# Kernel tuning notes

Measured on AMD Instinct MI355X. Metric: run time of the kernel, lower is better.

The kernel has to match this reference:

```python
import jax, jax.numpy as jnp
import numpy as np

EPS = 1e-6
ROPE_BASE = 10000.0


def layer_norm(x, scale, bias):
    mu = jnp.mean(x, axis=-1, keepdims=True)
    var = jnp.mean(jnp.square(x - mu), axis=-1, keepdims=True)
    return (x - mu) * jax.lax.rsqrt(var + EPS) * scale + bias


def make_rope(head_dim, seq_len):
    half = head_dim // 2
    inv_freq = 1.0 / (ROPE_BASE ** (jnp.arange(half, dtype=jnp.float32) / half))
    freqs = jnp.outer(jnp.arange(seq_len, dtype=jnp.float32), inv_freq)  # (T, half)
    cos = jnp.concatenate([jnp.cos(freqs), jnp.cos(freqs)], axis=-1)[:, None, :]  # (T,1,Dh)
    sin = jnp.concatenate([jnp.sin(freqs), jnp.sin(freqs)], axis=-1)[:, None, :]

    def rotate_half(x):
        x1, x2 = x[..., :half], x[..., half:]
        return jnp.concatenate([-x2, x1], axis=-1)

    def apply(q, k):
        return q * cos + rotate_half(q) * sin, k * cos + rotate_half(k) * sin
    return apply


def mha(x, Wq, bq, Wk, bk, Wv, bv, Wo, bo, causal, rope):
    # x: (..., S, D) -> (..., S, D)
    q = jnp.einsum('...sd,dhk->...shk', x, Wq) + bq
    k = jnp.einsum('...sd,dhk->...shk', x, Wk) + bk
    v = jnp.einsum('...sd,dhk->...shk', x, Wv) + bv
    if rope is not None:
        q, k = rope(q, k)
    scale = 1.0 / np.sqrt(q.shape[-1]).astype(np.float32)
    logits = jnp.einsum('...thk,...shk->...hts', q, k) * scale
    if causal:
        S = q.shape[-3]
        mask = jnp.tril(jnp.ones((S, S), dtype=jnp.bool_))
        logits = jnp.where(mask, logits, jnp.finfo(logits.dtype).min)
    probs = jax.nn.softmax(logits, axis=-1)
    o = jnp.einsum('...hts,...shk->...thk', probs, v)
    return jnp.einsum('...thk,hkd->...td', o, Wo) + bo


def setup_inputs() -> dict:
    key = jax.random.key(0)
    B, T, M, D, H, Dh, F = 8, 128, 16, 1024, 16, 64, 4096
    ks = jax.random.split(key, 12)
    s = 0.02
    return {
        'x': jax.random.normal(ks[0], (B, T, M, D), jnp.float32),
        'ln1_scale': jnp.ones((D,), jnp.float32), 'ln1_bias': jnp.zeros((D,), jnp.float32),
        't_Wq': jax.random.normal(ks[1], (D, H, Dh), jnp.float32) * s,
        't_bq': jnp.zeros((H, Dh), jnp.float32),
        't_Wk': jax.random.normal(ks[2], (D, H, Dh), jnp.float32) * s,
        't_bk': jnp.zeros((H, Dh), jnp.float32),
        't_Wv': jax.random.normal(ks[3], (D, H, Dh), jnp.float32) * s,
        't_bv': jnp.zeros((H, Dh), jnp.float32),
        't_Wo': jax.random.normal(ks[4], (H, Dh, D), jnp.float32) * s,
        't_bo': jnp.zeros((D,), jnp.float32),
        'ln2_scale': jnp.ones((D,), jnp.float32), 'ln2_bias': jnp.zeros((D,), jnp.float32),
        'm_Wq': jax.random.normal(ks[5], (D, H, Dh), jnp.float32) * s,
        'm_bq': jnp.zeros((H, Dh), jnp.float32),
        'm_Wk': jax.random.normal(ks[6], (D, H, Dh), jnp.float32) * s,
        'm_bk': jnp.zeros((H, Dh), jnp.float32),
        'm_Wv': jax.random.normal(ks[7], (D, H, Dh), jnp.float32) * s,
        'm_bv': jnp.zeros((H, Dh), jnp.float32),
        'm_Wo': jax.random.normal(ks[8], (H, Dh, D), jnp.float32) * s,
        'm_bo': jnp.zeros((D,), jnp.float32),
        'ln3_scale': jnp.ones((D,), jnp.float32), 'ln3_bias': jnp.zeros((D,), jnp.float32),
        'mlp_W1': jax.random.normal(ks[9], (D, F), jnp.float32) * s,
        'mlp_b1': jnp.zeros((F,), jnp.float32),
        'mlp_W2': jax.random.normal(ks[10], (F, D), jnp.float32) * s,
        'mlp_b2': jnp.zeros((D,), jnp.float32),
    }


def reference(x, ln1_scale, ln1_bias, t_Wq, t_bq, t_Wk, t_bk, t_Wv, t_bv, t_Wo, t_bo,
              ln2_scale, ln2_bias, m_Wq, m_bq, m_Wk, m_bk, m_Wv, m_bv, m_Wo, m_bo,
              ln3_scale, ln3_bias, mlp_W1, mlp_b1, mlp_W2, mlp_b2):
    # x: (B, T, M, D)
    T = x.shape[1]
    Dh = t_Wq.shape[-1]
    rope = make_rope(Dh, T)
    # --- temporal axial attention (causal, RoPE), M folded into batch ---
    h = layer_norm(x, ln1_scale, ln1_bias)
    h = jnp.swapaxes(h, 1, 2)  # (B, M, T, D)
    a = mha(h, t_Wq, t_bq, t_Wk, t_bk, t_Wv, t_bv, t_Wo, t_bo, causal=True, rope=rope)
    x = x + jnp.swapaxes(a, 1, 2)
    # --- modality axial attention (bidirectional, no RoPE), T folded into batch ---
    h = layer_norm(x, ln2_scale, ln2_bias)  # (B, T, M, D), M is seq axis
    x = x + mha(h, m_Wq, m_bq, m_Wk, m_bk, m_Wv, m_bv, m_Wo, m_bo, causal=False, rope=None)
    # --- MLP ---
    h = layer_norm(x, ln3_scale, ln3_bias)
    h = jax.nn.gelu(jnp.einsum('...d,df->...f', h, mlp_W1) + mlp_b1)
    x = x + jnp.einsum('...f,fd->...d', h, mlp_W2) + mlp_b2
    return x
```

## Files before the change

kernel.cpp:

```cpp
#include <hip/hip_runtime.h>
#include <stdint.h>

typedef __attribute__((ext_vector_type(8))) __bf16 bf16x8;
typedef __attribute__((ext_vector_type(4))) float f32x4;

#define DEV static __device__ __forceinline__

DEV unsigned short f2bf(float f) {
    unsigned int u = __float_as_uint(f);
    u = (u + 0x7fffu + ((u >> 16) & 1u)) >> 16;
    return (unsigned short)u;
}
DEV float bf2f(unsigned short h) { return __uint_as_float((unsigned int)h << 16); }

DEV void async_ld16(const void* g, void* l) {
    __builtin_amdgcn_global_load_lds(
        (const __attribute__((address_space(1))) void*)g,
        (__attribute__((address_space(3))) void*)l, 16, 0, 0);
}

DEV f32x4 mfma16(bf16x8 a, bf16x8 b, f32x4 c) {
    return __builtin_amdgcn_mfma_f32_16x16x32_bf16(a, b, c, 0, 0, 0);
}

DEV float gelu_f(float v) {
    float u = 0.7978845608028654f * (v + 0.044715f * v * v * v);
    u = fminf(fmaxf(u, -9.f), 9.f);
    const float e = __expf(2.f * u);
    const float th = (e - 1.f) / (e + 1.f);
    return 0.5f * v * (1.0f + th);
}

__global__ __launch_bounds__(256) void wconv_kernel(
    const float* __restrict__ src, unsigned short* __restrict__ dst, int K, int N)
{
    __shared__ float tile[32][33];
    const int tx = threadIdx.x & 31;
    const int ty = threadIdx.x >> 5;
    const long nb = blockIdx.x;
    const long kb = blockIdx.y;
#pragma unroll
    for (int i = 0; i < 32; i += 8)
        tile[ty + i][tx] = src[(kb * 32 + ty + i) * N + nb * 32 + tx];
    __syncthreads();
#pragma unroll
    for (int i = 0; i < 32; i += 8)
        dst[(nb * 32 + ty + i) * K + kb * 32 + tx] = f2bf(tile[tx][ty + i]);
}

__global__ void pack_bias_kernel(const float* __restrict__ bq, const float* __restrict__ bk,
                                 const float* __restrict__ bv, float* __restrict__ o)
{
    int i = blockIdx.x * 256 + threadIdx.x;
    if (i < 1024) o[i] = bq[i];
    else if (i < 2048) o[i] = bk[i - 1024];
    else if (i < 3072) o[i] = bv[i - 2048];
}

__global__ __launch_bounds__(256) void ln_kernel(
    const float* __restrict__ x, const float* __restrict__ scale,
    const float* __restrict__ bias, unsigned short* __restrict__ out)
{
    const int lane = threadIdx.x & 63;
    const int wave = threadIdx.x >> 6;
    const long tok = (long)blockIdx.x * 4 + wave;
    const float* xp = x + tok * 1024;
    float4 v[4];
    float sum = 0.f, sq = 0.f;
#pragma unroll
    for (int i = 0; i < 4; ++i) {
        v[i] = ((const float4*)xp)[i * 64 + lane];
        sum += v[i].x + v[i].y + v[i].z + v[i].w;
        sq += v[i].x * v[i].x + v[i].y * v[i].y + v[i].z * v[i].z + v[i].w * v[i].w;
    }
#pragma unroll
    for (int off = 1; off < 64; off <<= 1) {
        sum += __shfl_xor(sum, off);
        sq  += __shfl_xor(sq, off);
    }
    const float mu = sum * (1.f / 1024.f);
    const float var = sq * (1.f / 1024.f) - mu * mu;
    const float rs = rsqrtf(var + 1e-6f);
#pragma unroll
    for (int i = 0; i < 4; ++i) {
        const float4 sc = ((const float4*)scale)[i * 64 + lane];
        const float4 bi = ((const float4*)bias)[i * 64 + lane];
        ushort4 o;
        o.x = f2bf((v[i].x - mu) * rs * sc.x + bi.x);
        o.y = f2bf((v[i].y - mu) * rs * sc.y + bi.y);
        o.z = f2bf((v[i].z - mu) * rs * sc.z + bi.z);
        o.w = f2bf((v[i].w - mu) * rs * sc.w + bi.w);
        *(ushort4*)&out[tok * 1024 + (i * 64 + lane) * 4] = o;
    }
}

template <int EPI, bool ROPE>
__global__ __launch_bounds__(512, 2) void gemm256_kernel(
    const unsigned short* __restrict__ A, const unsigned short* __restrict__ Bt,
    const float* __restrict__ bias, const float* __restrict__ resid,
    void* __restrict__ Cout, int M, int N, int K, int nbx)
{
    __shared__ __align__(16) unsigned short lds[3][2][8192];
    const int tid = threadIdx.x;
    const int lane = tid & 63;
    const int wave = tid >> 6;
    const int wr = wave >> 2;
    const int wc = wave & 3;
    const int lr = lane & 15;
    const int hi = lane >> 4;

    const int nwg = gridDim.x;
    const int cpx = nwg >> 3;
    int bid = blockIdx.x;
    bid = (bid & 7) * cpx + (bid >> 3);
    const int bx = bid % nbx, by = bid / nbx;
    const long row0 = (long)by * 256;
    const long col0 = (long)bx * 256;
    const int NT = K >> 5;

    const int r_ = tid >> 2;
    const int pc = tid & 3;
    const int sxr = (r_ >> 1) & 3;
    const unsigned short* gA0 = A + (row0 + r_) * (long)K + (pc ^ sxr) * 8;
    const unsigned short* gA1 = A + (row0 + r_ + 128) * (long)K + (pc ^ sxr) * 8;
    const unsigned short* gB0 = Bt + (col0 + r_) * (long)K + (pc ^ sxr) * 8;
    const unsigned short* gB1 = Bt + (col0 + r_ + 128) * (long)K + (pc ^ sxr) * 8;

    auto stage = [&](int buf, int kt) {
        const long ko = (long)kt * 32;
        async_ld16(gA0 + ko, &lds[buf][0][tid * 8]);
        async_ld16(gA1 + ko, &lds[buf][0][tid * 8 + 4096]);
        async_ld16(gB0 + ko, &lds[buf][1][tid * 8]);
        async_ld16(gB1 + ko, &lds[buf][1][tid * 8 + 4096]);
    };

    int aoff[8], boff[4];
#pragma unroll
    for (int m = 0; m < 8; ++m) {
        const int row = wr * 128 + m * 16 + lr;
        aoff[m] = row * 64 + ((hi ^ ((row >> 1) & 3)) << 4);
    }
#pragma unroll
    for (int n = 0; n < 4; ++n) {
        const int row = wc * 64 + n * 16 + lr;
        boff[n] = row * 64 + ((hi ^ ((row >> 1) & 3)) << 4);
    }

    f32x4 acc[8][4];
#pragma unroll
    for (int i = 0; i < 8; ++i)
#pragma unroll
        for (int j = 0; j < 4; ++j) acc[i][j] = f32x4{0.f, 0.f, 0.f, 0.f};

    stage(0, 0);
    stage(1, 1);
    int cur = 0, sb = 2;

    for (int kt = 0; kt < NT; ++kt) {
        __builtin_amdgcn_sched_barrier(0);
        if (kt + 1 < NT) { asm volatile("s_waitcnt vmcnt(4)" ::: "memory"); }
        else             { asm volatile("s_waitcnt vmcnt(0)" ::: "memory"); }
        __builtin_amdgcn_sched_barrier(0);
        __builtin_amdgcn_s_barrier();
        __builtin_amdgcn_sched_barrier(0);

        if (kt + 2 < NT) stage(sb, kt + 2);
        __builtin_amdgcn_sched_barrier(0);

        const char* bA = (const char*)&lds[cur][0][0];
        const char* bB = (const char*)&lds[cur][1][0];
        bf16x8 a[8], b[4];
#pragma unroll
        for (int n = 0; n < 4; ++n) b[n] = *(const bf16x8*)(bB + boff[n]);
#pragma unroll
        for (int m = 0; m < 8; ++m) a[m] = *(const bf16x8*)(bA + aoff[m]);

        __builtin_amdgcn_s_setprio(1);
#pragma unroll
        for (int m = 0; m < 8; ++m)
#pragma unroll
            for (int n = 0; n < 4; ++n)
                acc[m][n] = mfma16(a[m], b[n], acc[m][n]);
        __builtin_amdgcn_s_setprio(0);

        __builtin_amdgcn_sched_barrier(0);
        __builtin_amdgcn_s_barrier();
        __builtin_amdgcn_sched_barrier(0);
        cur = (cur == 2) ? 0 : cur + 1;
        sb = (sb == 2) ? 0 : sb + 1;
    }

    __syncthreads();

    float bcol[4];
#pragma unroll
    for (int n = 0; n < 4; ++n) bcol[n] = bias[col0 + wc * 64 + n * 16 + lr];

    if (EPI == 2) {
        float (*eF)[256] = (float (*)[256])&lds[0][0][0];
        float* co = (float*)Cout;
#pragma unroll
        for (int q = 0; q < 4; ++q) {
            if (wr == (q >> 1)) {
                const int ib = (q & 1) * 4;
#pragma unroll
                for (int k2 = 0; k2 < 4; ++k2)
#pragma unroll
                    for (int n = 0; n < 4; ++n)
#pragma unroll
                        for (int j = 0; j < 4; ++j)
                            eF[k2 * 16 + hi * 4 + j][wc * 64 + n * 16 + lr] =
                                acc[ib + k2][n][j] + bcol[n];
            }
            __syncthreads();
#pragma unroll
            for (int it = 0; it < 8; ++it) {
                const int idx = it * 512 + tid;
                const int row = idx >> 6;
                const int ch = (idx & 63) * 4;
                const long g = row0 + q * 64 + row;
                float4 v = *(const float4*)&eF[row][ch];
                const float4 rv = *(const float4*)&resid[g * N + col0 + ch];
                v.x += rv.x; v.y += rv.y; v.z += rv.z; v.w += rv.w;
                *(float4*)&co[g * N + col0 + ch] = v;
            }
            __syncthreads();
        }
    } else {
        unsigned short (*eT)[256] = (unsigned short (*)[256])&lds[0][0][0];
        unsigned short* co = (unsigned short*)Cout;
        const bool doRope = ROPE && (col0 + wc * 64) < 2048;
#pragma unroll
        for (int h2 = 0; h2 < 2; ++h2) {
            if (wr == h2) {
                if (doRope) {
#pragma unroll
                    for (int i = 0; i < 8; ++i) {
                        const float t_i = (float)(int)(((row0 + h2 * 128 + i * 16) >> 4) & 127);
#pragma unroll
                        for (int n = 0; n < 2; ++n) {
                            const float dd = (float)(n * 16 + lr);
                            const float inv = __expf(dd * -0.2878231366242557f);
                            float sn, cs;
                            __sincosf(t_i * inv, &sn, &cs);
#pragma unroll
                            for (int j = 0; j < 4; ++j) {
                                const float lo = acc[i][n][j] + bcol[n];
                                const float hv = acc[i][n + 2][j] + bcol[n + 2];
                                eT[i * 16 + hi * 4 + j][wc * 64 + n * 16 + lr] = f2bf(lo * cs - hv * sn);
                                eT[i * 16 + hi * 4 + j][wc * 64 + 32 + n * 16 + lr] = f2bf(hv * cs + lo * sn);
                            }
                        }
                    }
                } else {
#pragma unroll
                    for (int i = 0; i < 8; ++i)
#pragma unroll
                        for (int n = 0; n < 4; ++n)
#pragma unroll
                            for (int j = 0; j < 4; ++j) {
                                float v = acc[i][n][j] + bcol[n];
                                if (EPI == 1) v = gelu_f(v);
                                eT[i * 16 + hi * 4 + j][wc * 64 + n * 16 + lr] = f2bf(v);
                            }
                }
            }
            __syncthreads();
#pragma unroll
            for (int it = 0; it < 8; ++it) {
                const int idx = it * 512 + tid;
                const int row = idx >> 5;
                const int ch = (idx & 31) * 8;
                *(uint4*)&co[(row0 + h2 * 128 + row) * N + col0 + ch] = *(const uint4*)&eT[row][ch];
            }
            __syncthreads();
        }
    }
}

__global__ __launch_bounds__(256) void attn_temporal(
    const unsigned short* __restrict__ qkv, unsigned short* __restrict__ out)
{
    const int bid = blockIdx.x;
    const int h = bid & 15;
    const int mm = (bid >> 4) & 15;
    const int b = bid >> 8;
    const int tid = threadIdx.x;
    const int lane = tid & 63;
    const int wave = tid >> 6;
    const int lr = lane & 15;
    const int lk = (lane >> 4) * 8;
    const int r4 = (lane >> 4) * 4;

    __shared__ __align__(16) unsigned short smemA[128 * 136];
    __shared__ __align__(16) unsigned short smemV[64 * 136];
    unsigned short (*Ks)[72] = (unsigned short (*)[72])smemA;
    unsigned short (*Ps)[136] = (unsigned short (*)[136])smemA;
    unsigned short (*Vt)[136] = (unsigned short (*)[136])smemV;

    const long tokbase = (long)b * 2048 + mm;

#pragma unroll
    for (int i = 0; i < 4; ++i) {
        const int cc = tid + 256 * i;
        const int s = cc >> 3, part = cc & 7;
        const unsigned short* g = qkv + (tokbase + s * 16l) * 3072 + 1024 + h * 64 + part * 8;
        *(uint4*)&Ks[s][part * 8] = *(const uint4*)g;
    }
#pragma unroll
    for (int i = 0; i < 4; ++i) {
        const int cc = tid + 256 * i;
        const int s = cc >> 3, part = cc & 7;
        const unsigned short* g = qkv + (tokbase + s * 16l) * 3072 + 2048 + h * 64 + part * 8;
        union { uint4 u; unsigned short us[8]; } uu;
        uu.u = *(const uint4*)g;
#pragma unroll
        for (int j = 0; j < 8; ++j) Vt[part * 8 + j][s] = uu.us[j];
    }
    __syncthreads();

    bf16x8 qf[2][2];
#pragma unroll
    for (int rb = 0; rb < 2; ++rb)
#pragma unroll
        for (int ks = 0; ks < 2; ++ks) {
            const int t = wave * 32 + rb * 16 + lr;
            qf[rb][ks] = *(const bf16x8*)(qkv + (tokbase + t * 16l) * 3072 + h * 64 + ks * 32 + lk);
        }

    f32x4 sacc[2][8];
#pragma unroll
    for (int rb = 0; rb < 2; ++rb)
#pragma unroll
        for (int cb = 0; cb < 8; ++cb) sacc[rb][cb] = f32x4{0.f, 0.f, 0.f, 0.f};

#pragma unroll
    for (int cb = 0; cb < 8; ++cb)
#pragma unroll
        for (int ks = 0; ks < 2; ++ks) {
            const bf16x8 kf = *(const bf16x8*)&Ks[cb * 16 + lr][ks * 32 + lk];
            sacc[0][cb] = mfma16(qf[0][ks], kf, sacc[0][cb]);
            sacc[1][cb] = mfma16(qf[1][ks], kf, sacc[1][cb]);
        }

    float recip[2][4];
#pragma unroll
    for (int rb = 0; rb < 2; ++rb)
#pragma unroll
        for (int r = 0; r < 4; ++r) {
            const int trow = wave * 32 + rb * 16 + r4 + r;
            float mx = -1e30f;
#pragma unroll
            for (int cb = 0; cb < 8; ++cb) {
                const int s = cb * 16 + lr;
                const float v = (s <= trow) ? sacc[rb][cb][r] * 0.125f : -1e30f;
                sacc[rb][cb][r] = v;
                mx = fmaxf(mx, v);
            }
            mx = fmaxf(mx, __shfl_xor(mx, 1));
            mx = fmaxf(mx, __shfl_xor(mx, 2));
            mx = fmaxf(mx, __shfl_xor(mx, 4));
            mx = fmaxf(mx, __shfl_xor(mx, 8));
            float sum = 0.f;
#pragma unroll
            for (int cb = 0; cb < 8; ++cb) {
                const float e = __expf(sacc[rb][cb][r] - mx);
                sacc[rb][cb][r] = e;
                sum += e;
            }
            sum += __shfl_xor(sum, 1);
            sum += __shfl_xor(sum, 2);
            sum += __shfl_xor(sum, 4);
            sum += __shfl_xor(sum, 8);
            recip[rb][r] = 1.f / sum;
        }
    __syncthreads();

#pragma unroll
    for (int rb = 0; rb < 2; ++rb)
#pragma unroll
        for (int cb = 0; cb < 8; ++cb)
#pragma unroll
            for (int r = 0; r < 4; ++r)
                Ps[wave * 32 + rb * 16 + r4 + r][cb * 16 + lr] = f2bf(sacc[rb][cb][r]);
    __syncthreads();

    f32x4 oacc[2][4];
#pragma unroll
    for (int rb = 0; rb < 2; ++rb)
#pragma unroll
        for (int cb = 0; cb < 4; ++cb) oacc[rb][cb] = f32x4{0.f, 0.f, 0.f, 0.f};

#pragma unroll
    for (int ks = 0; ks < 4; ++ks) {
        bf16x8 pf[2];
        pf[0] = *(const bf16x8*)&Ps[wave * 32 + lr][ks * 32 + lk];
        pf[1] = *(const bf16x8*)&Ps[wave * 32 + 16 + lr][ks * 32 + lk];
#pragma unroll
        for (int cb = 0; cb < 4; ++cb) {
            const bf16x8 vf = *(const bf16x8*)&Vt[cb * 16 + lr][ks * 32 + lk];
            oacc[0][cb] = mfma16(pf[0], vf, oacc[0][cb]);
            oacc[1][cb] = mfma16(pf[1], vf, oacc[1][cb]);
        }
    }

#pragma unroll
    for (int rb = 0; rb < 2; ++rb)
#pragma unroll
        for (int cb = 0; cb < 4; ++cb)
#pragma unroll
            for (int r = 0; r < 4; ++r) {
                const int trow = wave * 32 + rb * 16 + r4 + r;
                out[(tokbase + trow * 16l) * 1024 + h * 64 + cb * 16 + lr] =
                    f2bf(oacc[rb][cb][r] * recip[rb][r]);
            }
}

__global__ __launch_bounds__(256) void attn_modality(
    const unsigned short* __restrict__ qkv, unsigned short* __restrict__ out)
{
    const int tid = threadIdx.x;
    const int lane = tid & 63;
    const int wave = tid >> 6;
    const int lr = lane & 15;
    const int lk = (lane >> 4) * 8;
    const int r4 = (lane >> 4) * 4;
    const long base = (long)blockIdx.x * 16;

    __shared__ __align__(16) unsigned short smem[4][64 * 40 + 16 * 40];
    unsigned short (*Vt)[40] = (unsigned short (*)[40]) & smem[wave][0];
    unsigned short (*Pl)[40] = (unsigned short (*)[40]) & smem[wave][64 * 40];

    for (int i = lane; i < 400; i += 64)
        *(uint4*)&smem[wave][i * 8] = make_uint4(0u, 0u, 0u, 0u);

    for (int hi = 0; hi < 4; ++hi) {
        const int h = wave * 4 + hi;
#pragma unroll
        for (int i = 0; i < 2; ++i) {
            const int cc = lane + 64 * i;
            const int s = cc >> 3, d0 = (cc & 7) * 8;
            union { uint4 u; unsigned short us[8]; } uu;
            uu.u = *(const uint4*)(qkv + (base + s) * 3072 + 2048 + h * 64 + d0);
#pragma unroll
            for (int j = 0; j < 8; ++j) Vt[d0 + j][s] = uu.us[j];
        }
        bf16x8 qf[2], kf[2];
#pragma unroll
        for (int ks = 0; ks < 2; ++ks) {
            qf[ks] = *(const bf16x8*)(qkv + (base + lr) * 3072 + h * 64 + ks * 32 + lk);
            kf[ks] = *(const bf16x8*)(qkv + (base + lr) * 3072 + 1024 + h * 64 + ks * 32 + lk);
        }
        f32x4 sv = f32x4{0.f, 0.f, 0.f, 0.f};
        sv = mfma16(qf[0], kf[0], sv);
        sv = mfma16(qf[1], kf[1], sv);

        float recip[4], pe[4];
#pragma unroll
        for (int r = 0; r < 4; ++r) {
            const float v = sv[r] * 0.125f;
            float mx = v;
            mx = fmaxf(mx, __shfl_xor(mx, 1));
            mx = fmaxf(mx, __shfl_xor(mx, 2));
            mx = fmaxf(mx, __shfl_xor(mx, 4));
            mx = fmaxf(mx, __shfl_xor(mx, 8));
            const float e = __expf(v - mx);
            float sum = e;
            sum += __shfl_xor(sum, 1);
            sum += __shfl_xor(sum, 2);
            sum += __shfl_xor(sum, 4);
            sum += __shfl_xor(sum, 8);
            recip[r] = 1.f / sum;
            pe[r] = e;
        }
#pragma unroll
        for (int r = 0; r < 4; ++r) Pl[r4 + r][lr] = f2bf(pe[r]);

        const bf16x8 pf = *(const bf16x8*)&Pl[lr][lk];
#pragma unroll
        for (int cb = 0; cb < 4; ++cb) {
            const bf16x8 vf = *(const bf16x8*)&Vt[cb * 16 + lr][lk];
            f32x4 o = f32x4{0.f, 0.f, 0.f, 0.f};
            o = mfma16(pf, vf, o);
#pragma unroll
            for (int r = 0; r < 4; ++r)
                out[(base + r4 + r) * 1024 + h * 64 + cb * 16 + lr] = f2bf(o[r] * recip[r]);
        }
    }
}

extern "C" void kernel_launch(void* const* d_in, const int* in_sizes, int n_in,
                              void* d_out, int out_size, void* d_ws, size_t ws_size,
                              hipStream_t stream)
{
    (void)in_sizes; (void)n_in; (void)out_size;
    const float* x    = (const float*)d_in[0];
    const float* ln1s = (const float*)d_in[1];
    const float* ln1b = (const float*)d_in[2];
    const float* tWq  = (const float*)d_in[3];
    const float* tbq  = (const float*)d_in[4];
    const float* tWk  = (const float*)d_in[5];
    const float* tbk  = (const float*)d_in[6];
    const float* tWv  = (const float*)d_in[7];
    const float* tbv  = (const float*)d_in[8];
    const float* tWo  = (const float*)d_in[9];
    const float* tbo  = (const float*)d_in[10];
    const float* ln2s = (const float*)d_in[11];
    const float* ln2b = (const float*)d_in[12];
    const float* mWq  = (const float*)d_in[13];
    const float* mbq  = (const float*)d_in[14];
    const float* mWk  = (const float*)d_in[15];
    const float* mbk  = (const float*)d_in[16];
    const float* mWv  = (const float*)d_in[17];
    const float* mbv  = (const float*)d_in[18];
    const float* mWo  = (const float*)d_in[19];
    const float* mbo  = (const float*)d_in[20];
    const float* ln3s = (const float*)d_in[21];
    const float* ln3b = (const float*)d_in[22];
    const float* W1   = (const float*)d_in[23];
    const float* b1   = (const float*)d_in[24];
    const float* W2   = (const float*)d_in[25];
    const float* b2   = (const float*)d_in[26];

    if (ws_size < 201351168ull) return;

    char* ws = (char*)d_ws;
    unsigned short* Wt_tqkv = (unsigned short*)(ws + 0);
    unsigned short* Wt_to   = (unsigned short*)(ws + 6291456);
    unsigned short* Wt_mqkv = (unsigned short*)(ws + 8388608);
    unsigned short* Wt_mo   = (unsigned short*)(ws + 14680064);
    unsigned short* Wt1     = (unsigned short*)(ws + 16777216);
    unsigned short* Wt2     = (unsigned short*)(ws + 25165824);
    float* bias_t           = (float*)(ws + 33554432);
    float* bias_m           = (float*)(ws + 33566720);
    unsigned short* act     = (unsigned short*)(ws + 33579008);
    unsigned short* qkv     = (unsigned short*)(ws + 67133440);
    unsigned short* hidden  = qkv;
    float* xout = (float*)d_out;

    dim3 blk(256);
    dim3 blk5(512);

    wconv_kernel<<<dim3(32, 32), blk, 0, stream>>>(tWq, Wt_tqkv, 1024, 1024);
    wconv_kernel<<<dim3(32, 32), blk, 0, stream>>>(tWk, Wt_tqkv + 1024 * 1024, 1024, 1024);
    wconv_kernel<<<dim3(32, 32), blk, 0, stream>>>(tWv, Wt_tqkv + 2048 * 1024, 1024, 1024);
    wconv_kernel<<<dim3(32, 32), blk, 0, stream>>>(tWo, Wt_to, 1024, 1024);
    wconv_kernel<<<dim3(32, 32), blk, 0, stream>>>(mWq, Wt_mqkv, 1024, 1024);
    wconv_kernel<<<dim3(32, 32), blk, 0, stream>>>(mWk, Wt_mqkv + 1024 * 1024, 1024, 1024);
    wconv_kernel<<<dim3(32, 32), blk, 0, stream>>>(mWv, Wt_mqkv + 2048 * 1024, 1024, 1024);
    wconv_kernel<<<dim3(32, 32), blk, 0, stream>>>(mWo, Wt_mo, 1024, 1024);
    wconv_kernel<<<dim3(128, 32), blk, 0, stream>>>(W1, Wt1, 1024, 4096);
    wconv_kernel<<<dim3(32, 128), blk, 0, stream>>>(W2, Wt2, 4096, 1024);
    pack_bias_kernel<<<12, blk, 0, stream>>>(tbq, tbk, tbv, bias_t);
    pack_bias_kernel<<<12, blk, 0, stream>>>(mbq, mbk, mbv, bias_m);

    ln_kernel<<<4096, blk, 0, stream>>>(x, ln1s, ln1b, act);
    gemm256_kernel<0, true><<<768, blk5, 0, stream>>>(act, Wt_tqkv, bias_t, nullptr, qkv, 16384, 3072, 1024, 12);
    attn_temporal<<<2048, blk, 0, stream>>>(qkv, act);
    gemm256_kernel<2, false><<<256, blk5, 0, stream>>>(act, Wt_to, tbo, x, xout, 16384, 1024, 1024, 4);
    ln_kernel<<<4096, blk, 0, stream>>>(xout, ln2s, ln2b, act);
    gemm256_kernel<0, false><<<768, blk5, 0, stream>>>(act, Wt_mqkv, bias_m, nullptr, qkv, 16384, 3072, 1024, 12);
    attn_modality<<<1024, blk, 0, stream>>>(qkv, act);
    gemm256_kernel<2, false><<<256, blk5, 0, stream>>>(act, Wt_mo, mbo, xout, xout, 16384, 1024, 1024, 4);
    ln_kernel<<<4096, blk, 0, stream>>>(xout, ln3s, ln3b, act);
    gemm256_kernel<1, false><<<1024, blk5, 0, stream>>>(act, Wt1, b1, nullptr, hidden, 16384, 4096, 1024, 16);
    gemm256_kernel<2, false><<<256, blk5, 0, stream>>>(hidden, Wt2, b2, xout, xout, 16384, 1024, 4096, 4);
}
```

Measured before the change: 825.6 us.

## Shrink GEMM tiles to 128x128 with 256 threads and double buffering

Replaces the 256x256 GEMM tile (512 threads, triple-buffered LDS) with a 128x128 tile on 4 waves using a two-stage LDS pipeline, and launches four times as many workgroups. The goal is more workgroups per GPU and better load balance on small-N GEMMs (the 256-workgroup N=1024 GEMMs barely cover the CUs). The trade-off is lower arithmetic intensity per tile, so more global/L2 traffic per FLOP, and a shallower prefetch pipeline that can expose load latency. The epilogues and RoPE indexing are rewritten for the new tile shape.

Result: slower. 861.1 us (median of 3 runs) (+4.3%).

```diff
diff --git a/kernel.cpp b/kernel.cpp
--- a/kernel.cpp
+++ b/kernel.cpp
@@ -95,17 +95,17 @@
 }
 
 template <int EPI, bool ROPE>
-__global__ __launch_bounds__(512, 2) void gemm256_kernel(
+__global__ __launch_bounds__(256, 3) void gemm128_kernel(
     const unsigned short* __restrict__ A, const unsigned short* __restrict__ Bt,
     const float* __restrict__ bias, const float* __restrict__ resid,
     void* __restrict__ Cout, int M, int N, int K, int nbx)
 {
-    __shared__ __align__(16) unsigned short lds[3][2][8192];
+    __shared__ __align__(16) unsigned short lds[2][2][4096];
     const int tid = threadIdx.x;
     const int lane = tid & 63;
     const int wave = tid >> 6;
-    const int wr = wave >> 2;
-    const int wc = wave & 3;
+    const int wr = wave >> 1;
+    const int wc = wave & 1;
     const int lr = lane & 15;
     const int hi = lane >> 4;
 
@@ -114,30 +114,30 @@
     int bid = blockIdx.x;
     bid = (bid & 7) * cpx + (bid >> 3);
     const int bx = bid % nbx, by = bid / nbx;
-    const long row0 = (long)by * 256;
-    const long col0 = (long)bx * 256;
+    const long row0 = (long)by * 128;
+    const long col0 = (long)bx * 128;
     const int NT = K >> 5;
 
     const int r_ = tid >> 2;
     const int pc = tid & 3;
     const int sxr = (r_ >> 1) & 3;
     const unsigned short* gA0 = A + (row0 + r_) * (long)K + (pc ^ sxr) * 8;
-    const unsigned short* gA1 = A + (row0 + r_ + 128) * (long)K + (pc ^ sxr) * 8;
+    const unsigned short* gA1 = A + (row0 + r_ + 64) * (long)K + (pc ^ sxr) * 8;
     const unsigned short* gB0 = Bt + (col0 + r_) * (long)K + (pc ^ sxr) * 8;
-    const unsigned short* gB1 = Bt + (col0 + r_ + 128) * (long)K + (pc ^ sxr) * 8;
+    const unsigned short* gB1 = Bt + (col0 + r_ + 64) * (long)K + (pc ^ sxr) * 8;
 
     auto stage = [&](int buf, int kt) {
         const long ko = (long)kt * 32;
         async_ld16(gA0 + ko, &lds[buf][0][tid * 8]);
-        async_ld16(gA1 + ko, &lds[buf][0][tid * 8 + 4096]);
+        async_ld16(gA1 + ko, &lds[buf][0][tid * 8 + 2048]);
         async_ld16(gB0 + ko, &lds[buf][1][tid * 8]);
-        async_ld16(gB1 + ko, &lds[buf][1][tid * 8 + 4096]);
+        async_ld16(gB1 + ko, &lds[buf][1][tid * 8 + 2048]);
     };
 
-    int aoff[8], boff[4];
-#pragma unroll
-    for (int m = 0; m < 8; ++m) {
-        const int row = wr * 128 + m * 16 + lr;
+    int aoff[4], boff[4];
+#pragma unroll
+    for (int m = 0; m < 4; ++m) {
+        const int row = wr * 64 + m * 16 + lr;
         aoff[m] = row * 64 + ((hi ^ ((row >> 1) & 3)) << 4);
     }
 #pragma unroll
@@ -146,17 +146,17 @@
         boff[n] = row * 64 + ((hi ^ ((row >> 1) & 3)) << 4);
     }
 
-    f32x4 acc[8][4];
-#pragma unroll
-    for (int i = 0; i < 8; ++i)
+    f32x4 acc[4][4];
+#pragma unroll
+    for (int i = 0; i < 4; ++i)
 #pragma unroll
         for (int j = 0; j < 4; ++j) acc[i][j] = f32x4{0.f, 0.f, 0.f, 0.f};
 
     stage(0, 0);
-    stage(1, 1);
-    int cur = 0, sb = 2;
 
     for (int kt = 0; kt < NT; ++kt) {
+        const int b = kt & 1;
+        if (kt + 1 < NT) stage(b ^ 1, kt + 1);
         __builtin_amdgcn_sched_barrier(0);
         if (kt + 1 < NT) { asm volatile("s_waitcnt vmcnt(4)" ::: "memory"); }
         else             { asm volatile("s_waitcnt vmcnt(0)" ::: "memory"); }
@@ -164,30 +164,25 @@
         __builtin_amdgcn_s_barrier();
         __builtin_amdgcn_sched_barrier(0);
 
-        if (kt + 2 < NT) stage(sb, kt + 2);
-        __builtin_amdgcn_sched_barrier(0);
-
-        const char* bA = (const char*)&lds[cur][0][0];
-        const char* bB = (const char*)&lds[cur][1][0];
-        bf16x8 a[8], b[4];
-#pragma unroll
-        for (int n = 0; n < 4; ++n) b[n] = *(const bf16x8*)(bB + boff[n]);
-#pragma unroll
-        for (int m = 0; m < 8; ++m) a[m] = *(const bf16x8*)(bA + aoff[m]);
+        const char* bA = (const char*)&lds[b][0][0];
+        const char* bB = (const char*)&lds[b][1][0];
+        bf16x8 a[4], bf[4];
+#pragma unroll
+        for (int n = 0; n < 4; ++n) bf[n] = *(const bf16x8*)(bB + boff[n]);
+#pragma unroll
+        for (int m = 0; m < 4; ++m) a[m] = *(const bf16x8*)(bA + aoff[m]);
 
         __builtin_amdgcn_s_setprio(1);
 #pragma unroll
-        for (int m = 0; m < 8; ++m)
+        for (int m = 0; m < 4; ++m)
 #pragma unroll
             for (int n = 0; n < 4; ++n)
-                acc[m][n] = mfma16(a[m], b[n], acc[m][n]);
+                acc[m][n] = mfma16(a[m], bf[n], acc[m][n]);
         __builtin_amdgcn_s_setprio(0);
 
         __builtin_amdgcn_sched_barrier(0);
         __builtin_amdgcn_s_barrier();
         __builtin_amdgcn_sched_barrier(0);
-        cur = (cur == 2) ? 0 : cur + 1;
-        sb = (sb == 2) ? 0 : sb + 1;
     }
 
     __syncthreads();
@@ -197,28 +192,27 @@
     for (int n = 0; n < 4; ++n) bcol[n] = bias[col0 + wc * 64 + n * 16 + lr];
 
     if (EPI == 2) {
-        float (*eF)[256] = (float (*)[256])&lds[0][0][0];
+        float (*eF)[128] = (float (*)[128])&lds[0][0][0];
         float* co = (float*)Cout;
 #pragma unroll
-        for (int q = 0; q < 4; ++q) {
-            if (wr == (q >> 1)) {
-                const int ib = (q & 1) * 4;
-#pragma unroll
-                for (int k2 = 0; k2 < 4; ++k2)
+        for (int half = 0; half < 2; ++half) {
+            if (wr == half) {
+#pragma unroll
+                for (int m = 0; m < 4; ++m)
 #pragma unroll
                     for (int n = 0; n < 4; ++n)
 #pragma unroll
                         for (int j = 0; j < 4; ++j)
-                            eF[k2 * 16 + hi * 4 + j][wc * 64 + n * 16 + lr] =
-                                acc[ib + k2][n][j] + bcol[n];
+                            eF[m * 16 + hi * 4 + j][wc * 64 + n * 16 + lr] =
+                                acc[m][n][j] + bcol[n];
             }
             __syncthreads();
 #pragma unroll
             for (int it = 0; it < 8; ++it) {
-                const int idx = it * 512 + tid;
-                const int row = idx >> 6;
-                const int ch = (idx & 63) * 4;
-                const long g = row0 + q * 64 + row;
+                const int idx = it * 256 + tid;
+                const int row = idx >> 5;
+                const int ch = (idx & 31) * 4;
+                const long g = row0 + half * 64 + row;
                 float4 v = *(const float4*)&eF[row][ch];
                 const float4 rv = *(const float4*)&resid[g * N + col0 + ch];
                 v.x += rv.x; v.y += rv.y; v.z += rv.z; v.w += rv.w;
@@ -227,53 +221,47 @@
             __syncthreads();
         }
     } else {
-        unsigned short (*eT)[256] = (unsigned short (*)[256])&lds[0][0][0];
+        unsigned short (*eT)[128] = (unsigned short (*)[128])&lds[0][0][0];
         unsigned short* co = (unsigned short*)Cout;
         const bool doRope = ROPE && (col0 + wc * 64) < 2048;
-#pragma unroll
-        for (int h2 = 0; h2 < 2; ++h2) {
-            if (wr == h2) {
-                if (doRope) {
-#pragma unroll
-                    for (int i = 0; i < 8; ++i) {
-                        const float t_i = (float)(int)(((row0 + h2 * 128 + i * 16) >> 4) & 127);
-#pragma unroll
-                        for (int n = 0; n < 2; ++n) {
-                            const float dd = (float)(n * 16 + lr);
-                            const float inv = __expf(dd * -0.2878231366242557f);
-                            float sn, cs;
-                            __sincosf(t_i * inv, &sn, &cs);
-#pragma unroll
-                            for (int j = 0; j < 4; ++j) {
-                                const float lo = acc[i][n][j] + bcol[n];
-                                const float hv = acc[i][n + 2][j] + bcol[n + 2];
-                                eT[i * 16 + hi * 4 + j][wc * 64 + n * 16 + lr] = f2bf(lo * cs - hv * sn);
-                                eT[i * 16 + hi * 4 + j][wc * 64 + 32 + n * 16 + lr] = f2bf(hv * cs + lo * sn);
-                            }
-                        }
+        if (doRope) {
+#pragma unroll
+            for (int m = 0; m < 4; ++m) {
+                const float t_i = (float)(int)(((row0 + wr * 64 + m * 16) >> 4) & 127);
+#pragma unroll
+                for (int n = 0; n < 2; ++n) {
+                    const float dd = (float)(n * 16 + lr);
+                    const float inv = __expf(dd * -0.2878231366242557f);
+                    float sn, cs;
+                    __sincosf(t_i * inv, &sn, &cs);
+#pragma unroll
+                    for (int j = 0; j < 4; ++j) {
+                        const float lo = acc[m][n][j] + bcol[n];
+                        const float hv = acc[m][n + 2][j] + bcol[n + 2];
+                        eT[wr * 64 + m * 16 + hi * 4 + j][wc * 64 + n * 16 + lr] = f2bf(lo * cs - hv * sn);
+                        eT[wr * 64 + m * 16 + hi * 4 + j][wc * 64 + 32 + n * 16 + lr] = f2bf(hv * cs + lo * sn);
                     }
-                } else {
-#pragma unroll
-                    for (int i = 0; i < 8; ++i)
-#pragma unroll
-                        for (int n = 0; n < 4; ++n)
-#pragma unroll
-                            for (int j = 0; j < 4; ++j) {
-                                float v = acc[i][n][j] + bcol[n];
-                                if (EPI == 1) v = gelu_f(v);
-                                eT[i * 16 + hi * 4 + j][wc * 64 + n * 16 + lr] = f2bf(v);
-                            }
                 }
             }
-            __syncthreads();
-#pragma unroll
-            for (int it = 0; it < 8; ++it) {
-                const int idx = it * 512 + tid;
-                const int row = idx >> 5;
-                const int ch = (idx & 31) * 8;
-                *(uint4*)&co[(row0 + h2 * 128 + row) * N + col0 + ch] = *(const uint4*)&eT[row][ch];
-            }
-            __syncthreads();
+        } else {
+#pragma unroll
+            for (int m = 0; m < 4; ++m)
+#pragma unroll
+                for (int n = 0; n < 4; ++n)
+#pragma unroll
+                    for (int j = 0; j < 4; ++j) {
+                        float v = acc[m][n][j] + bcol[n];
+                        if (EPI == 1) v = gelu_f(v);
+                        eT[wr * 64 + m * 16 + hi * 4 + j][wc * 64 + n * 16 + lr] = f2bf(v);
+                    }
+        }
+        __syncthreads();
+#pragma unroll
+        for (int it = 0; it < 8; ++it) {
+            const int idx = it * 256 + tid;
+            const int row = idx >> 4;
+            const int ch = (idx & 15) * 8;
+            *(uint4*)&co[(row0 + row) * N + col0 + ch] = *(const uint4*)&eT[row][ch];
         }
     }
 }
@@ -539,7 +527,6 @@
     float* xout = (float*)d_out;
 
     dim3 blk(256);
-    dim3 blk5(512);
 
     wconv_kernel<<<dim3(32, 32), blk, 0, stream>>>(tWq, Wt_tqkv, 1024, 1024);
     wconv_kernel<<<dim3(32, 32), blk, 0, stream>>>(tWk, Wt_tqkv + 1024 * 1024, 1024, 1024);
@@ -555,14 +542,14 @@
     pack_bias_kernel<<<12, blk, 0, stream>>>(mbq, mbk, mbv, bias_m);
 
     ln_kernel<<<4096, blk, 0, stream>>>(x, ln1s, ln1b, act);
-    gemm256_kernel<0, true><<<768, blk5, 0, stream>>>(act, Wt_tqkv, bias_t, nullptr, qkv, 16384, 3072, 1024, 12);
+    gemm128_kernel<0, true><<<3072, blk, 0, stream>>>(act, Wt_tqkv, bias_t, nullptr, qkv, 16384, 3072, 1024, 24);
     attn_temporal<<<2048, blk, 0, stream>>>(qkv, act);
-    gemm256_kernel<2, false><<<256, blk5, 0, stream>>>(act, Wt_to, tbo, x, xout, 16384, 1024, 1024, 4);
+    gemm128_kernel<2, false><<<1024, blk, 0, stream>>>(act, Wt_to, tbo, x, xout, 16384, 1024, 1024, 8);
     ln_kernel<<<4096, blk, 0, stream>>>(xout, ln2s, ln2b, act);
-    gemm256_kernel<0, false><<<768, blk5, 0, stream>>>(act, Wt_mqkv, bias_m, nullptr, qkv, 16384, 3072, 1024, 12);
+    gemm128_kernel<0, false><<<3072, blk, 0, stream>>>(act, Wt_mqkv, bias_m, nullptr, qkv, 16384, 3072, 1024, 24);
     attn_modality<<<1024, blk, 0, stream>>>(qkv, act);
-    gemm256_kernel<2, false><<<256, blk5, 0, stream>>>(act, Wt_mo, mbo, xout, xout, 16384, 1024, 1024, 4);
+    gemm128_kernel<2, false><<<1024, blk, 0, stream>>>(act, Wt_mo, mbo, xout, xout, 16384, 1024, 1024, 8);
     ln_kernel<<<4096, blk, 0, stream>>>(xout, ln3s, ln3b, act);
-    gemm256_kernel<1, false><<<1024, blk5, 0, stream>>>(act, Wt1, b1, nullptr, hidden, 16384, 4096, 1024, 16);
-    gemm256_kernel<2, false><<<256, blk5, 0, stream>>>(hidden, Wt2, b2, xout, xout, 16384, 1024, 4096, 4);
-}
+    gemm128_kernel<1, false><<<4096, blk, 0, stream>>>(act, Wt1, b1, nullptr, hidden, 16384, 4096, 1024, 32);
+    gemm128_kernel<2, false><<<1024, blk, 0, stream>>>(hidden, Wt2, b2, xout, xout, 16384, 1024, 4096, 8);
+}
```
